# Optimization experiments

Hardware: AMD Instinct MI355X
Metric: run time of the kernel (lower is better)

The kernel has to match this reference:

```python
import jax, jax.numpy as jnp
import numpy as np

B, T, S, N, C, H = 2, 16, 256, 32, 3072, 24
D = C // H  # 128 head_dim
EPS = 1e-6


def _layernorm(x):
    # LayerNorm, elementwise_affine=False, eps=1e-6
    mu = jnp.mean(x, axis=-1, keepdims=True)
    var = jnp.mean(jnp.square(x - mu), axis=-1, keepdims=True)
    return (x - mu) * jax.lax.rsqrt(var + EPS)


def _rmsnorm(x, w):
    # RMSNorm with learnable weight, computed in fp32 (matches x.float() path)
    ms = jnp.mean(jnp.square(x), axis=-1, keepdims=True)
    return x * jax.lax.rsqrt(ms + EPS) * w


def setup_inputs() -> dict:
    key = jax.random.key(0)
    ks = jax.random.split(key, 8)
    f = lambda k, sh: jax.random.normal(k, sh, dtype=jnp.float32)
    sc = 1.0 / np.sqrt(C)
    return {
        "x": f(ks[0], (B, T * S, C)),
        "motion_vec": f(ks[1], (B, T, N, C)),
        "motion_mask": jax.random.uniform(ks[2], (B, T * S), dtype=jnp.float32),
        "w_kv": f(ks[3], (2 * C, C)) * sc,
        "b_kv": jnp.zeros((2 * C,), jnp.float32),
        "w_q": f(ks[4], (C, C)) * sc,
        "b_q": jnp.zeros((C,), jnp.float32),
        "w_o": f(ks[5], (C, C)) * sc,
        "b_o": jnp.zeros((C,), jnp.float32),
        "q_norm_w": jnp.ones((D,), jnp.float32),
        "k_norm_w": jnp.ones((D,), jnp.float32),
    }


def reference(x, motion_vec, motion_mask, w_kv, b_kv, w_q, b_q, w_o, b_o,
              q_norm_w, k_norm_w):
    x_motion = _layernorm(motion_vec)            # [B,T,N,C]
    x_feat = _layernorm(x)                       # [B,T*S,C]

    kv = x_motion @ w_kv.T + b_kv                # [B,T,N,2C]
    kv = kv.reshape(B, T, N, 2, H, D)
    k, v = kv[:, :, :, 0], kv[:, :, :, 1]        # [B,T,N,H,D]

    q = (x_feat @ w_q.T + b_q).reshape(B, T, S, H, D)
    q = _rmsnorm(q, q_norm_w)
    k = _rmsnorm(k, k_norm_w)

    # frame-local cross-attention: queries = spatial tokens, keys = motion tokens
    scale = 1.0 / jnp.sqrt(jnp.float32(D))
    scores = jnp.einsum('btshd,btnhd->bthsn', q, k) * scale  # [B,T,H,S,N]
    probs = jax.nn.softmax(scores, axis=-1)
    attn = jnp.einsum('bthsn,btnhd->btshd', probs, v)        # [B,T,S,H,D]
    attn = attn.reshape(B, T * S, C)

    out = attn @ w_o.T + b_o                     # [B,T*S,C]
    return out * motion_mask[:, :, None]
```

## Files before the change

kernel.cpp:

```cpp
#include <hip/hip_runtime.h>
#include <math.h>

typedef unsigned short u16;
typedef unsigned int u32;
typedef short bf16x8 __attribute__((ext_vector_type(8)));
typedef float f32x4 __attribute__((ext_vector_type(4)));
typedef u16 u16x4 __attribute__((ext_vector_type(4)));
typedef u16 u16x8 __attribute__((ext_vector_type(8)));
typedef u32 u32x4 __attribute__((ext_vector_type(4)));

static __device__ __forceinline__ float b2f(u16 u) {
  union { u32 i; float f; } v; v.i = ((u32)u) << 16; return v.f;
}
static __device__ __forceinline__ u16 f2b(float f) {
  union { float f; u32 i; } v; v.f = f;
  u32 r = v.i + 0x7fffu + ((v.i >> 16) & 1u);
  return (u16)(r >> 16);
}
static __device__ __forceinline__ void cvt16(const float* src, u16* dst, int i) {
  f32x4 v = *(const f32x4*)(src + (size_t)i * 4);
  u16x4 w; w.x = f2b(v.x); w.y = f2b(v.y); w.z = f2b(v.z); w.w = f2b(v.w);
  *(u16x4*)(dst + (size_t)i * 4) = w;
}

static __device__ __forceinline__ void g2l16(const void* g, void* l) {
  typedef __attribute__((address_space(1))) const void gvoid;
  typedef __attribute__((address_space(3))) void lvoid;
  __builtin_amdgcn_global_load_lds((gvoid*)g, (lvoid*)l, 16, 0, 0);
}

__global__ __launch_bounds__(256)
void wcvt_kernel(const float* __restrict__ src, u16* __restrict__ dst, int n4)
{
  for (int i = blockIdx.x * 256 + threadIdx.x; i < n4; i += gridDim.x * 256)
    cvt16(src, dst, i);
}

__global__ __launch_bounds__(256)
void prep_kernel(const float* __restrict__ x, const float* __restrict__ mv,
                 u16* __restrict__ xf, u16* __restrict__ xm,
                 const float* __restrict__ wq, u16* __restrict__ wqs,
                 const float* __restrict__ wkv, u16* __restrict__ wkvs)
{
  const int b = blockIdx.x, tid = threadIdx.x;
  if (b >= 9216) {
    if (b < 10240) {
      const int n4 = 3072 * 3072 / 4;
      for (int i = (b - 9216) * 256 + tid; i < n4; i += 1024 * 256) cvt16(wq, wqs, i);
    } else {
      const int n4 = 6144 * 3072 / 4;
      for (int i = (b - 10240) * 256 + tid; i < n4; i += 1024 * 256) cvt16(wkv, wkvs, i);
    }
    return;
  }
  const float* src; u16* dst;
  if (b < 8192) { src = x + (size_t)b * 3072;          dst = xf + (size_t)b * 3072; }
  else          { src = mv + (size_t)(b - 8192) * 3072; dst = xm + (size_t)(b - 8192) * 3072; }

  f32x4 vals[3];
  #pragma unroll
  for (int i = 0; i < 3; ++i) vals[i] = *(const f32x4*)(src + tid * 4 + i * 1024);

  float s1 = 0.f, s2 = 0.f;
  #pragma unroll
  for (int i = 0; i < 3; ++i) {
    f32x4 v = vals[i];
    s1 += v.x + v.y + v.z + v.w;
    s2 += v.x * v.x + v.y * v.y + v.z * v.z + v.w * v.w;
  }
  #pragma unroll
  for (int o = 32; o > 0; o >>= 1) { s1 += __shfl_down(s1, o); s2 += __shfl_down(s2, o); }
  __shared__ float r1[4], r2[4];
  const int wv = tid >> 6, ln = tid & 63;
  if (ln == 0) { r1[wv] = s1; r2[wv] = s2; }
  __syncthreads();
  const float t1 = r1[0] + r1[1] + r1[2] + r1[3];
  const float t2 = r2[0] + r2[1] + r2[2] + r2[3];
  const float mu = t1 * (1.f / 3072.f);
  const float rs = rsqrtf(t2 * (1.f / 3072.f) - mu * mu + 1e-6f);
  #pragma unroll
  for (int i = 0; i < 3; ++i) {
    f32x4 v = vals[i]; u16x4 w;
    w.x = f2b((v.x - mu) * rs); w.y = f2b((v.y - mu) * rs);
    w.z = f2b((v.z - mu) * rs); w.w = f2b((v.w - mu) * rs);
    *(u16x4*)(dst + tid * 4 + i * 1024) = w;
  }
}

template<int EPI, typename TOUT>
static __device__ __forceinline__ void g256_body(
    const u16* __restrict__ A, const u16* __restrict__ Wb,
    const float* __restrict__ bias, const float* __restrict__ mask,
    TOUT* __restrict__ C, int N, int K, int tb, u16* L)
{
  const int tid = threadIdx.x, wave = tid >> 6, lane = tid & 63;
  const int nbx = N >> 7;
  const int brow = (tb / nbx) << 8;
  const int bcol = (tb % nbx) << 7;
  const int wr = wave >> 1, wc = wave & 1;

  const u16* gA = A + (size_t)brow * K;
  const u16* gB = Wb + (size_t)bcol * K;

  const int srow = tid >> 2;
  const int scol = 8 * ((lane & 3) ^ ((lane >> 3) & 3));
  const int rcoff = 8 * ((lane >> 4) ^ ((lane >> 1) & 3));

  f32x4 acc[8][4] = {};

  auto STAGE = [&](int b, int tk) {
    u16* bufA = &L[b * 12288];
    u16* bufB = bufA + 8192;
    const u16* srcA = gA + tk + scol;
    const u16* srcB = gB + tk + scol;
    #pragma unroll
    for (int j = 0; j < 4; ++j)
      g2l16(srcA + (size_t)(j * 64 + srow) * K, bufA + (j * 64 + wave * 16) * 32);
    #pragma unroll
    for (int j = 0; j < 2; ++j)
      g2l16(srcB + (size_t)(j * 64 + srow) * K, bufB + (j * 64 + wave * 16) * 32);
  };

  auto COMPUTE = [&](int b) {
    const u16* bufA = &L[b * 12288];
    const u16* bufB = bufA + 8192;
    bf16x8 af[8], bfv[4];
    #pragma unroll
    for (int m = 0; m < 8; ++m)
      af[m] = *(const bf16x8*)&bufA[(wr * 128 + m * 16 + (lane & 15)) * 32 + rcoff];
    #pragma unroll
    for (int n = 0; n < 4; ++n)
      bfv[n] = *(const bf16x8*)&bufB[(wc * 64 + n * 16 + (lane & 15)) * 32 + rcoff];
    __builtin_amdgcn_s_setprio(1);
    #pragma unroll
    for (int m = 0; m < 8; ++m)
      #pragma unroll
      for (int n = 0; n < 4; ++n)
        acc[m][n] = __builtin_amdgcn_mfma_f32_16x16x32_bf16(af[m], bfv[n], acc[m][n], 0, 0, 0);
    __builtin_amdgcn_s_setprio(0);
  };

  STAGE(0, 0);
  STAGE(1, 32);
  asm volatile("s_waitcnt vmcnt(6)" ::: "memory");
  __builtin_amdgcn_s_barrier();
  __builtin_amdgcn_sched_barrier(0);

  const int NT = K >> 5;
  int cur = 0;
  for (int t = 0; t < NT; ++t) {
    const bool pf = (t + 2) < NT;
    if (pf) {
      int nb = cur + 2; if (nb >= 3) nb -= 3;
      STAGE(nb, (t + 2) << 5);
    }
    COMPUTE(cur);
    if (pf) asm volatile("s_waitcnt vmcnt(6)" ::: "memory");
    else    asm volatile("s_waitcnt vmcnt(0)" ::: "memory");
    __builtin_amdgcn_s_barrier();
    __builtin_amdgcn_sched_barrier(0);
    if (++cur == 3) cur = 0;
  }

  #pragma unroll
  for (int m = 0; m < 8; ++m) {
    const int row = brow + wr * 128 + m * 16 + ((lane >> 4) << 2);
    #pragma unroll
    for (int n = 0; n < 4; ++n) {
      const int col = bcol + wc * 64 + n * 16 + (lane & 15);
      const float bv = bias[col];
      #pragma unroll
      for (int i = 0; i < 4; ++i) {
        float v = acc[m][n][i] + bv;
        if (EPI == 1) v *= mask[row + i];
        if constexpr (__is_same(TOUT, u16))
          C[(size_t)(row + i) * N + col] = f2b(v);
        else
          C[(size_t)(row + i) * N + col] = v;
      }
    }
  }
}

template<int EPI, typename TOUT>
__global__ __launch_bounds__(256, 2)
void gemm256(const u16* __restrict__ A, const u16* __restrict__ Wb,
             const float* __restrict__ bias, const float* __restrict__ mask,
             TOUT* __restrict__ C, int M, int N, int K)
{
  __shared__ __align__(16) u16 L[36864];
  const int nwg = gridDim.x;
  const int tb = (blockIdx.x & 7) * (nwg >> 3) + (blockIdx.x >> 3);
  g256_body<EPI, TOUT>(A, Wb, bias, mask, C, N, K, tb, L);
}

__global__ __launch_bounds__(256, 2)
void gemm_fused(const u16* __restrict__ Aq, const u16* __restrict__ Bq,
                const float* __restrict__ bq, u16* __restrict__ Cq,
                const u16* __restrict__ Akv, const u16* __restrict__ Bkv,
                const float* __restrict__ bkv, u16* __restrict__ Ckv, int K)
{
  __shared__ __align__(16) u16 L[36864];
  const int b0 = blockIdx.x;
  if (b0 < 768) {
    const int tb = (b0 & 7) * 96 + (b0 >> 3);
    g256_body<0, u16>(Aq, Bq, bq, nullptr, Cq, 3072, K, tb, L);
  } else {
    const int b2 = b0 - 768;
    const int tb = (b2 & 7) * 24 + (b2 >> 3);
    g256_body<0, u16>(Akv, Bkv, bkv, nullptr, Ckv, 6144, K, tb, L);
  }
}

template<int EPI, typename TOUT>
__global__ __launch_bounds__(256, 2)
void gemm192(const u16* __restrict__ A, const u16* __restrict__ Wb,
             const float* __restrict__ bias, const float* __restrict__ mask,
             TOUT* __restrict__ C, int M, int N, int K)
{
  __shared__ __align__(16) u16 L[30720];
  const int tid = threadIdx.x, wave = tid >> 6, lane = tid & 63;
  const int nwg = gridDim.x;
  const int tb = (blockIdx.x & 7) * (nwg >> 3) + (blockIdx.x >> 3);
  const int nbx = N / 192;
  const int brow = (tb / nbx) << 7;
  const int bcol = (tb % nbx) * 192;
  const int wr = wave >> 1, wc = wave & 1;

  const u16* gA = A + (size_t)brow * K;
  const u16* gB = Wb + (size_t)bcol * K;

  const int srow = tid >> 2;
  const int scol = 8 * ((lane & 3) ^ ((lane >> 3) & 3));
  const int rcoff = 8 * ((lane >> 4) ^ ((lane >> 1) & 3));
  const int lr = lane & 15;

  f32x4 acc[4][6] = {};

  auto STAGE = [&](int b, int tk) {
    u16* bufA = &L[b * 10240];
    u16* bufB = bufA + 4096;
    const u16* srcA = gA + tk + scol;
    const u16* srcB = gB + tk + scol;
    #pragma unroll
    for (int j = 0; j < 2; ++j)
      g2l16(srcA + (size_t)(j * 64 + srow) * K, bufA + (j * 64 + wave * 16) * 32);
    #pragma unroll
    for (int j = 0; j < 3; ++j)
      g2l16(srcB + (size_t)(j * 64 + srow) * K, bufB + (j * 64 + wave * 16) * 32);
  };

  auto COMPUTE = [&](int b) {
    const u16* bufA = &L[b * 10240];
    const u16* bufB = bufA + 4096;
    bf16x8 af[4], bfv[6];
    #pragma unroll
    for (int m = 0; m < 4; ++m)
      af[m] = *(const bf16x8*)&bufA[(wr * 64 + m * 16 + lr) * 32 + rcoff];
    #pragma unroll
    for (int n = 0; n < 6; ++n)
      bfv[n] = *(const bf16x8*)&bufB[(wc * 96 + n * 16 + lr) * 32 + rcoff];
    __builtin_amdgcn_s_setprio(1);
    #pragma unroll
    for (int m = 0; m < 4; ++m)
      #pragma unroll
      for (int n = 0; n < 6; ++n)
        acc[m][n] = __builtin_amdgcn_mfma_f32_16x16x32_bf16(af[m], bfv[n], acc[m][n], 0, 0, 0);
    __builtin_amdgcn_s_setprio(0);
  };

  STAGE(0, 0);
  STAGE(1, 32);
  asm volatile("s_waitcnt vmcnt(5)" ::: "memory");
  __builtin_amdgcn_s_barrier();
  __builtin_amdgcn_sched_barrier(0);

  const int NT = K >> 5;
  int cur = 0;
  for (int t = 0; t < NT; ++t) {
    const bool pf = (t + 2) < NT;
    if (pf) {
      int nb = cur + 2; if (nb >= 3) nb -= 3;
      STAGE(nb, (t + 2) << 5);
    }
    COMPUTE(cur);
    if (pf) asm volatile("s_waitcnt vmcnt(5)" ::: "memory");
    else    asm volatile("s_waitcnt vmcnt(0)" ::: "memory");
    __builtin_amdgcn_s_barrier();
    __builtin_amdgcn_sched_barrier(0);
    if (++cur == 3) cur = 0;
  }

  #pragma unroll
  for (int m = 0; m < 4; ++m) {
    const int row = brow + wr * 64 + m * 16 + ((lane >> 4) << 2);
    #pragma unroll
    for (int n = 0; n < 6; ++n) {
      const int col = bcol + wc * 96 + n * 16 + lr;
      const float bv = bias[col];
      #pragma unroll
      for (int i = 0; i < 4; ++i) {
        float v = acc[m][n][i] + bv;
        if (EPI == 1) v *= mask[row + i];
        if constexpr (__is_same(TOUT, u16))
          C[(size_t)(row + i) * N + col] = f2b(v);
        else
          C[(size_t)(row + i) * N + col] = v;
      }
    }
  }
}

template<int EPI, typename TOUT>
__global__ __launch_bounds__(256)
void gemm_mixed(const u16* __restrict__ A, const float* __restrict__ W,
                const float* __restrict__ bias, const float* __restrict__ mask,
                TOUT* __restrict__ C, int M, int N, int K)
{
  __shared__ __align__(16) u16 lA[4096];
  __shared__ __align__(16) u16 lB[4096];
  const int tid = threadIdx.x, wave = tid >> 6, lane = tid & 63;
  const int nbx = N >> 7;
  const int brow = (blockIdx.x / nbx) << 7;
  const int bcol = (blockIdx.x % nbx) << 7;
  const int wr = wave >> 1, wc = wave & 1;

  f32x4 acc[4][4] = {};
  const u16* gA = A + (size_t)brow * K;
  const float* gB = W + (size_t)bcol * K;
  const int br = tid >> 1, bk0 = (tid & 1) << 4;
  const float* bsrc0 = gB + (size_t)br * K + bk0;
  u16* bdst = &lB[br * 32 + bk0];

  for (int tk = 0; tk < K; tk += 32) {
    #pragma unroll
    for (int j = 0; j < 2; ++j) {
      const int c = j * 256 + wave * 64 + lane;
      const int r = c >> 2, k8 = (c & 3) << 3;
      g2l16(gA + (size_t)r * K + tk + k8, (char*)lA + (size_t)(j * 256 + wave * 64) * 16);
    }
    {
      const float* src = bsrc0 + tk;
      #pragma unroll
      for (int j = 0; j < 4; ++j) {
        f32x4 v = *(const f32x4*)(src + 4 * j);
        u16x4 w; w.x = f2b(v.x); w.y = f2b(v.y); w.z = f2b(v.z); w.w = f2b(v.w);
        *(u16x4*)(bdst + 4 * j) = w;
      }
    }
    __syncthreads();

    bf16x8 af[4], bfr[4];
    #pragma unroll
    for (int m = 0; m < 4; ++m)
      af[m] = *(const bf16x8*)&lA[(wr * 64 + m * 16 + (lane & 15)) * 32 + ((lane >> 4) << 3)];
    #pragma unroll
    for (int n = 0; n < 4; ++n)
      bfr[n] = *(const bf16x8*)&lB[(wc * 64 + n * 16 + (lane & 15)) * 32 + ((lane >> 4) << 3)];
    #pragma unroll
    for (int m = 0; m < 4; ++m)
      #pragma unroll
      for (int n = 0; n < 4; ++n)
        acc[m][n] = __builtin_amdgcn_mfma_f32_16x16x32_bf16(af[m], bfr[n], acc[m][n], 0, 0, 0);
    __syncthreads();
  }

  #pragma unroll
  for (int m = 0; m < 4; ++m) {
    const int row = brow + wr * 64 + m * 16 + ((lane >> 4) << 2);
    #pragma unroll
    for (int n = 0; n < 4; ++n) {
      const int col = bcol + wc * 64 + n * 16 + (lane & 15);
      const float bv = bias[col];
      #pragma unroll
      for (int i = 0; i < 4; ++i) {
        float v = acc[m][n][i] + bv;
        if (EPI == 1) v *= mask[row + i];
        if constexpr (__is_same(TOUT, u16))
          C[(size_t)(row + i) * N + col] = f2b(v);
        else
          C[(size_t)(row + i) * N + col] = v;
      }
    }
  }
}

__global__ __launch_bounds__(256)
void attn_wcvt(const u16* __restrict__ qb, const u16* __restrict__ kvb,
               const float* __restrict__ qw, const float* __restrict__ kw,
               u16* __restrict__ attnb,
               const float* __restrict__ wo, u16* __restrict__ wos)
{
  __shared__ __align__(16) u16 Kn[32 * 136];
  __shared__ __align__(16) u16 Vt[128 * 40];
  __shared__ __align__(16) u16 Pl[256 * 40];
  __shared__ __align__(16) u16 Ol[4][16 * 136];
  const int tid = threadIdx.x;
  if (blockIdx.x >= 768) {
    const int n4 = 3072 * 3072 / 4;
    for (int i = (blockIdx.x - 768) * 256 + tid; i < n4; i += 1024 * 256)
      cvt16(wo, wos, i);
    return;
  }
  const int wave = tid >> 6, lane = tid & 63;
  const int h = blockIdx.x % 24;
  const int bt = blockIdx.x / 24;

  {
    const int n = tid >> 3, sub = tid & 7;
    const size_t base = (size_t)(bt * 32 + n) * 6144 + (size_t)h * 128;
    const u16* kp = kvb + base + sub * 16;
    u16x8 k0 = *(const u16x8*)kp;
    u16x8 k1 = *(const u16x8*)(kp + 8);
    float kv_[16]; float ss = 0.f;
    #pragma unroll
    for (int j = 0; j < 8; ++j) { kv_[j] = b2f(k0[j]); kv_[8 + j] = b2f(k1[j]); }
    #pragma unroll
    for (int j = 0; j < 16; ++j) ss += kv_[j] * kv_[j];
    ss += __shfl_xor(ss, 1); ss += __shfl_xor(ss, 2); ss += __shfl_xor(ss, 4);
    const float krs = rsqrtf(ss * (1.f / 128.f) + 1e-6f);
    u16x8 w0, w1;
    #pragma unroll
    for (int j = 0; j < 8; ++j) {
      const int d = sub * 16 + j;
      w0[j] = f2b(kv_[j] * krs * kw[d] * qw[d]);
      w1[j] = f2b(kv_[8 + j] * krs * kw[d + 8] * qw[d + 8]);
    }
    *(u16x8*)&Kn[n * 136 + sub * 16] = w0;
    *(u16x8*)&Kn[n * 136 + sub * 16 + 8] = w1;
  }
  {
    const int k = tid >> 3, dc = (tid & 7) * 16;
    const u16* vp = kvb + (size_t)(bt * 32 + k) * 6144 + (size_t)h * 128 + 3072 + dc;
    u16x8 v0 = *(const u16x8*)vp;
    u16x8 v1 = *(const u16x8*)(vp + 8);
    #pragma unroll
    for (int j = 0; j < 8; ++j) {
      Vt[(dc + j) * 40 + k] = v0[j];
      Vt[(dc + 8 + j) * 40 + k] = v1[j];
    }
  }
  __syncthreads();

  const int q0 = wave * 64;
  const int lr = lane & 15, lg = lane >> 4;

  for (int m = 0; m < 4; ++m) {
    const int qrow = q0 + m * 16 + lr;
    const u16* qp = qb + (size_t)(bt * 256 + qrow) * 3072 + (size_t)h * 128 + lg * 8;
    bf16x8 qf[4];
    #pragma unroll
    for (int k = 0; k < 4; ++k) qf[k] = *(const bf16x8*)(qp + k * 32);
    float ss = 0.f;
    #pragma unroll
    for (int k = 0; k < 4; ++k)
      #pragma unroll
      for (int j = 0; j < 8; ++j) { const float f = b2f((u16)qf[k][j]); ss += f * f; }
    ss += __shfl_xor(ss, 16); ss += __shfl_xor(ss, 32);
    const float qsc = rsqrtf(ss * (1.f / 128.f) + 1e-6f) * 0.08838834764831845f;
    #pragma unroll
    for (int k = 0; k < 4; ++k)
      #pragma unroll
      for (int j = 0; j < 8; ++j)
        qf[k][j] = (short)f2b(b2f((u16)qf[k][j]) * qsc);

    f32x4 s0 = {0.f, 0.f, 0.f, 0.f}, s1 = {0.f, 0.f, 0.f, 0.f};
    #pragma unroll
    for (int k = 0; k < 4; ++k) {
      bf16x8 kb0 = *(const bf16x8*)&Kn[(lr) * 136 + k * 32 + lg * 8];
      bf16x8 kb1 = *(const bf16x8*)&Kn[(16 + lr) * 136 + k * 32 + lg * 8];
      s0 = __builtin_amdgcn_mfma_f32_16x16x32_bf16(qf[k], kb0, s0, 0, 0, 0);
      s1 = __builtin_amdgcn_mfma_f32_16x16x32_bf16(qf[k], kb1, s1, 0, 0, 0);
    }

    float mx[4], sm[4], e0[4], e1[4];
    #pragma unroll
    for (int i = 0; i < 4; ++i) mx[i] = fmaxf(s0[i], s1[i]);
    #pragma unroll
    for (int o = 1; o <= 8; o <<= 1)
      #pragma unroll
      for (int i = 0; i < 4; ++i) mx[i] = fmaxf(mx[i], __shfl_xor(mx[i], o));
    #pragma unroll
    for (int i = 0; i < 4; ++i) {
      e0[i] = __expf(s0[i] - mx[i]);
      e1[i] = __expf(s1[i] - mx[i]);
      sm[i] = e0[i] + e1[i];
    }
    #pragma unroll
    for (int o = 1; o <= 8; o <<= 1)
      #pragma unroll
      for (int i = 0; i < 4; ++i) sm[i] += __shfl_xor(sm[i], o);
    #pragma unroll
    for (int i = 0; i < 4; ++i) {
      const float inv = 1.f / sm[i];
      const int pr = (q0 + m * 16 + lg * 4 + i) * 40;
      Pl[pr + lr] = f2b(e0[i] * inv);
      Pl[pr + 16 + lr] = f2b(e1[i] * inv);
    }
    asm volatile("s_waitcnt lgkmcnt(0)" ::: "memory");
    __builtin_amdgcn_sched_barrier(0);

    bf16x8 pf = *(const bf16x8*)&Pl[(q0 + m * 16 + lr) * 40 + lg * 8];
    f32x4 o_[8];
    #pragma unroll
    for (int n = 0; n < 8; ++n) {
      bf16x8 vb = *(const bf16x8*)&Vt[(n * 16 + lr) * 40 + lg * 8];
      o_[n] = __builtin_amdgcn_mfma_f32_16x16x32_bf16(
                pf, vb, (f32x4){0.f, 0.f, 0.f, 0.f}, 0, 0, 0);
    }

    u16* ow = &Ol[wave][0];
    #pragma unroll
    for (int n = 0; n < 8; ++n)
      #pragma unroll
      for (int i = 0; i < 4; ++i)
        ow[(lg * 4 + i) * 136 + n * 16 + lr] = f2b(o_[n][i]);
    asm volatile("s_waitcnt lgkmcnt(0)" ::: "memory");
    __builtin_amdgcn_sched_barrier(0);
    const int r = lane >> 2, cc = (lane & 3) * 32;
    u16* gout = attnb + (size_t)(bt * 256 + q0 + m * 16 + r) * 3072 + (size_t)h * 128 + cc;
    #pragma unroll
    for (int c = 0; c < 4; ++c)
      *(u16x8*)(gout + c * 8) = *(const u16x8*)&ow[r * 136 + cc + c * 8];
    asm volatile("s_waitcnt lgkmcnt(0)" ::: "memory");
    __builtin_amdgcn_sched_barrier(0);
  }
}

extern "C" void kernel_launch(void* const* d_in, const int* in_sizes, int n_in,
                              void* d_out, int out_size, void* d_ws, size_t ws_size,
                              hipStream_t stream) {
  const float* x    = (const float*)d_in[0];
  const float* mv   = (const float*)d_in[1];
  const float* mask = (const float*)d_in[2];
  const float* wkv  = (const float*)d_in[3];
  const float* bkv  = (const float*)d_in[4];
  const float* wq   = (const float*)d_in[5];
  const float* bq   = (const float*)d_in[6];
  const float* wo   = (const float*)d_in[7];
  const float* bo   = (const float*)d_in[8];
  const float* qnw  = (const float*)d_in[9];
  const float* knw  = (const float*)d_in[10];
  float* out = (float*)d_out;

  char* ws = (char*)d_ws;

  if (ws_size >= 176160768u) {
    u16* wqs  = (u16*)(ws);
    u16* wkvs = (u16*)(ws + 18874368);
    u16* xf   = (u16*)(ws + 56623104);
    u16* xm   = (u16*)(ws + 106954752);
    u16* qbuf = (u16*)(ws + 113246208);
    u16* kvb  = (u16*)(ws + 163577856);
    u16* wos  = wqs;

    prep_kernel<<<11264, 256, 0, stream>>>(x, mv, xf, xm, wq, wqs, wkv, wkvs);
    gemm_fused<<<960, 256, 0, stream>>>(xf, wqs, bq, qbuf, xm, wkvs, bkv, kvb, 3072);
    attn_wcvt<<<1792, 256, 0, stream>>>(qbuf, kvb, qnw, knw, xf, wo, wos);
    gemm192<1, float><<<1024, 256, 0, stream>>>(xf, wos, bo, mask, out, 8192, 3072, 3072);
  } else if (ws_size >= 157286400u) {
    u16* xf    = (u16*)(ws);
    u16* xm    = (u16*)(ws + 50331648);
    u16* qbuf  = (u16*)(ws + 56623104);
    u16* kvb   = (u16*)(ws + 106954752);
    u16* wslab = (u16*)(ws + 119537664);

    prep_kernel<<<9216, 256, 0, stream>>>(x, mv, xf, xm, wq, wslab, wkv, wslab);
    wcvt_kernel<<<2048, 256, 0, stream>>>(wq, wslab, 3072 * 3072 / 4);
    gemm256<0, u16><<<768, 256, 0, stream>>>(xf, wslab, bq, nullptr, qbuf, 8192, 3072, 3072);
    wcvt_kernel<<<2048, 256, 0, stream>>>(wkv, wslab, 6144 * 3072 / 4);
    gemm256<0, u16><<<192, 256, 0, stream>>>(xm, wslab, bkv, nullptr, kvb, 1024, 6144, 3072);
    attn_wcvt<<<768, 256, 0, stream>>>(qbuf, kvb, qnw, knw, xf, wo, wslab);
    wcvt_kernel<<<2048, 256, 0, stream>>>(wo, wslab, 3072 * 3072 / 4);
    gemm192<1, float><<<1024, 256, 0, stream>>>(xf, wslab, bo, mask, out, 8192, 3072, 3072);
  } else {
    u16* xf   = (u16*)(ws);
    u16* xm   = (u16*)(ws + 50331648);
    u16* qbuf = (u16*)(ws + 56623104);
    u16* kvb  = (u16*)(ws + 106954752);

    prep_kernel<<<9216, 256, 0, stream>>>(x, mv, xf, xm, wq, xf, wkv, xf);
    gemm_mixed<0, u16><<<1536, 256, 0, stream>>>(xf, wq, bq, nullptr, qbuf, 8192, 3072, 3072);
    gemm_mixed<0, u16><<<384, 256, 0, stream>>>(xm, wkv, bkv, nullptr, kvb, 1024, 6144, 3072);
    attn_wcvt<<<768, 256, 0, stream>>>(qbuf, kvb, qnw, knw, xf, wo, xf);
    gemm_mixed<1, float><<<1536, 256, 0, stream>>>(xf, wo, bo, mask, out, 8192, 3072, 3072);
  }
}
```

Before: 462.1 us.

## Add 8-wave 256x256 GEMM with ping-pong LDS pipeline for Q and output projections

Adds a new 512-thread GEMM kernel that computes 256x256 output tiles with 64-wide K steps and double-buffered LDS. Each K step is split into eight barrier-separated MFMA phases, and global prefetch is interleaved between them. It replaces the fused Q/KV GEMM and the 192-wide output GEMM, so the KV projection now launches as its own gemm256 kernel. The goals are more reuse per tile and better overlap of loads with MFMA; the costs are lower occupancy (one 128KB-LDS block per CU), many more barriers, and an extra kernel launch.

After: 496.7 us. 1.07x slower.

```diff
diff --git a/kernel.cpp b/kernel.cpp
--- a/kernel.cpp
+++ b/kernel.cpp
@@ -88,86 +88,139 @@
 }
 
 template<int EPI, typename TOUT>
-static __device__ __forceinline__ void g256_body(
-    const u16* __restrict__ A, const u16* __restrict__ Wb,
-    const float* __restrict__ bias, const float* __restrict__ mask,
-    TOUT* __restrict__ C, int N, int K, int tb, u16* L)
+__global__ __launch_bounds__(512, 1)
+void gemm8p(const u16* __restrict__ A, const u16* __restrict__ Wb,
+            const float* __restrict__ bias, const float* __restrict__ mask,
+            TOUT* __restrict__ C, int M, int N, int K)
 {
+  __shared__ __align__(16) u16 L[65536];
   const int tid = threadIdx.x, wave = tid >> 6, lane = tid & 63;
-  const int nbx = N >> 7;
-  const int brow = (tb / nbx) << 8;
-  const int bcol = (tb % nbx) << 7;
-  const int wr = wave >> 1, wc = wave & 1;
+  const int wr = wave >> 2, wc = wave & 3;
+  const int lr = lane & 15, lg = lane >> 4;
+
+  const int nwg = gridDim.x;
+  const int bid = (blockIdx.x & 7) * (nwg >> 3) + (blockIdx.x >> 3);
+  const int nbx = N >> 8;
+  const int brow = (bid / nbx) << 8;
+  const int bcol = (bid % nbx) << 8;
 
   const u16* gA = A + (size_t)brow * K;
   const u16* gB = Wb + (size_t)bcol * K;
 
-  const int srow = tid >> 2;
-  const int scol = 8 * ((lane & 3) ^ ((lane >> 3) & 3));
-  const int rcoff = 8 * ((lane >> 4) ^ ((lane >> 1) & 3));
+  const int sr = tid >> 3;
+  const int sc = 8 * ((tid & 7) ^ (sr & 7));
+  const int ch0 = 8 * (lg ^ (lr & 7));
+  const int ch1 = 8 * ((4 + lg) ^ (lr & 7));
 
   f32x4 acc[8][4] = {};
 
-  auto STAGE = [&](int b, int tk) {
-    u16* bufA = &L[b * 12288];
-    u16* bufB = bufA + 8192;
-    const u16* srcA = gA + tk + scol;
-    const u16* srcB = gB + tk + scol;
-    #pragma unroll
-    for (int j = 0; j < 4; ++j)
-      g2l16(srcA + (size_t)(j * 64 + srow) * K, bufA + (j * 64 + wave * 16) * 32);
-    #pragma unroll
-    for (int j = 0; j < 2; ++j)
-      g2l16(srcB + (size_t)(j * 64 + srow) * K, bufB + (j * 64 + wave * 16) * 32);
+  auto SG = [&](int sel, int d, int h, int T) {
+    const u16* g = (sel == 0 ? gA : gB) + (size_t)(h * 128 + sr) * K + T * 64 + sc;
+    u16* l = &L[sel * 32768 + (d * 2 + h) * 8192 + tid * 8];
+    g2l16(g, l);
+    g2l16(g + (size_t)64 * K, l + 4096);
   };
-
-  auto COMPUTE = [&](int b) {
-    const u16* bufA = &L[b * 12288];
-    const u16* bufB = bufA + 8192;
-    bf16x8 af[8], bfv[4];
-    #pragma unroll
-    for (int m = 0; m < 8; ++m)
-      af[m] = *(const bf16x8*)&bufA[(wr * 128 + m * 16 + (lane & 15)) * 32 + rcoff];
-    #pragma unroll
-    for (int n = 0; n < 4; ++n)
-      bfv[n] = *(const bf16x8*)&bufB[(wc * 64 + n * 16 + (lane & 15)) * 32 + rcoff];
-    __builtin_amdgcn_s_setprio(1);
-    #pragma unroll
-    for (int m = 0; m < 8; ++m)
-      #pragma unroll
-      for (int n = 0; n < 4; ++n)
-        acc[m][n] = __builtin_amdgcn_mfma_f32_16x16x32_bf16(af[m], bfv[n], acc[m][n], 0, 0, 0);
-    __builtin_amdgcn_s_setprio(0);
+  auto LDA = [&](int d, int mh, bf16x8 a[4][2]) {
+    const u16* base = &L[(d * 2 + wr) * 8192 + mh * 4096 + lr * 64];
+    #pragma unroll
+    for (int mm = 0; mm < 4; ++mm) {
+      a[mm][0] = *(const bf16x8*)&base[mm * 1024 + ch0];
+      a[mm][1] = *(const bf16x8*)&base[mm * 1024 + ch1];
+    }
   };
-
-  STAGE(0, 0);
-  STAGE(1, 32);
-  asm volatile("s_waitcnt vmcnt(6)" ::: "memory");
+  auto LDB = [&](int d, int nh, bf16x8 b[2][2]) {
+    const u16* base = &L[32768 + (d * 2 + (wc >> 1)) * 8192 + (wc & 1) * 4096 + nh * 2048 + lr * 64];
+    #pragma unroll
+    for (int nn = 0; nn < 2; ++nn) {
+      b[nn][0] = *(const bf16x8*)&base[nn * 1024 + ch0];
+      b[nn][1] = *(const bf16x8*)&base[nn * 1024 + ch1];
+    }
+  };
+
+#define MM8P(mh, nh, a, b)                                                     \
+  __builtin_amdgcn_s_setprio(1);                                               \
+  _Pragma("unroll")                                                            \
+  for (int mm = 0; mm < 4; ++mm)                                               \
+    _Pragma("unroll")                                                          \
+    for (int nn = 0; nn < 2; ++nn) {                                           \
+      acc[(mh)*4+mm][(nh)*2+nn] = __builtin_amdgcn_mfma_f32_16x16x32_bf16(     \
+          a[mm][0], b[nn][0], acc[(mh)*4+mm][(nh)*2+nn], 0, 0, 0);             \
+      acc[(mh)*4+mm][(nh)*2+nn] = __builtin_amdgcn_mfma_f32_16x16x32_bf16(     \
+          a[mm][1], b[nn][1], acc[(mh)*4+mm][(nh)*2+nn], 0, 0, 0);             \
+    }                                                                          \
+  __builtin_amdgcn_s_setprio(0);
+
+#define BAR_PRE()                                                              \
+  asm volatile("" ::: "memory");                                               \
+  __builtin_amdgcn_s_barrier();                                                \
+  asm volatile("s_waitcnt lgkmcnt(0)" ::: "memory");                           \
+  __builtin_amdgcn_sched_barrier(0);
+
+#define BAR_POST()                                                             \
+  asm volatile("" ::: "memory");                                               \
+  __builtin_amdgcn_s_barrier();                                                \
+  __builtin_amdgcn_sched_barrier(0);
+
+  SG(0, 0, 0, 0); SG(0, 0, 1, 0); SG(1, 0, 0, 0); SG(1, 0, 1, 0);
+  SG(0, 1, 0, 1);
+  asm volatile("s_waitcnt vmcnt(2)" ::: "memory");
   __builtin_amdgcn_s_barrier();
   __builtin_amdgcn_sched_barrier(0);
 
-  const int NT = K >> 5;
-  int cur = 0;
-  for (int t = 0; t < NT; ++t) {
-    const bool pf = (t + 2) < NT;
-    if (pf) {
-      int nb = cur + 2; if (nb >= 3) nb -= 3;
-      STAGE(nb, (t + 2) << 5);
-    }
-    COMPUTE(cur);
-    if (pf) asm volatile("s_waitcnt vmcnt(6)" ::: "memory");
-    else    asm volatile("s_waitcnt vmcnt(0)" ::: "memory");
-    __builtin_amdgcn_s_barrier();
-    __builtin_amdgcn_sched_barrier(0);
-    if (++cur == 3) cur = 0;
-  }
+  const int NI = K >> 7;
+  for (int i = 0; i < NI; ++i) {
+    const int t = 2 * i;
+    const bool pf = (i + 1) < NI;
+    bf16x8 a[4][2], b[2][2];
+
+    LDA(0, 0, a); LDB(0, 0, b);
+    SG(0, 1, 1, t + 1);
+    BAR_PRE(); MM8P(0, 0, a, b); BAR_POST();
+
+    LDB(0, 1, b);
+    SG(1, 1, 0, t + 1);
+    BAR_PRE(); MM8P(0, 1, a, b); BAR_POST();
+
+    LDA(0, 1, a);
+    SG(1, 1, 1, t + 1);
+    BAR_PRE(); MM8P(1, 1, a, b); BAR_POST();
+
+    LDB(0, 0, b);
+    if (pf) SG(0, 0, 0, t + 2);
+    BAR_PRE(); MM8P(1, 0, a, b);
+    if (pf) { asm volatile("s_waitcnt vmcnt(2)" ::: "memory"); }
+    else    { asm volatile("s_waitcnt vmcnt(0)" ::: "memory"); }
+    BAR_POST();
+
+    LDA(1, 0, a); LDB(1, 0, b);
+    if (pf) SG(0, 0, 1, t + 2);
+    BAR_PRE(); MM8P(0, 0, a, b); BAR_POST();
+
+    LDB(1, 1, b);
+    if (pf) SG(1, 0, 0, t + 2);
+    BAR_PRE(); MM8P(0, 1, a, b); BAR_POST();
+
+    LDA(1, 1, a);
+    if (pf) SG(1, 0, 1, t + 2);
+    BAR_PRE(); MM8P(1, 1, a, b); BAR_POST();
+
+    LDB(1, 0, b);
+    if (pf) SG(0, 1, 0, t + 3);
+    BAR_PRE(); MM8P(1, 0, a, b);
+    if (pf) { asm volatile("s_waitcnt vmcnt(2)" ::: "memory"); }
+    BAR_POST();
+  }
+
+#undef MM8P
+#undef BAR_PRE
+#undef BAR_POST
 
   #pragma unroll
   for (int m = 0; m < 8; ++m) {
-    const int row = brow + wr * 128 + m * 16 + ((lane >> 4) << 2);
+    const int row = brow + wr * 128 + m * 16 + (lg << 2);
     #pragma unroll
     for (int n = 0; n < 4; ++n) {
-      const int col = bcol + wc * 64 + n * 16 + (lane & 15);
+      const int col = bcol + wc * 64 + n * 16 + lr;
       const float bv = bias[col];
       #pragma unroll
       for (int i = 0; i < 4; ++i) {
@@ -189,42 +242,13 @@
              TOUT* __restrict__ C, int M, int N, int K)
 {
   __shared__ __align__(16) u16 L[36864];
+  const int tid = threadIdx.x, wave = tid >> 6, lane = tid & 63;
+
   const int nwg = gridDim.x;
-  const int tb = (blockIdx.x & 7) * (nwg >> 3) + (blockIdx.x >> 3);
-  g256_body<EPI, TOUT>(A, Wb, bias, mask, C, N, K, tb, L);
-}
-
-__global__ __launch_bounds__(256, 2)
-void gemm_fused(const u16* __restrict__ Aq, const u16* __restrict__ Bq,
-                const float* __restrict__ bq, u16* __restrict__ Cq,
-                const u16* __restrict__ Akv, const u16* __restrict__ Bkv,
-                const float* __restrict__ bkv, u16* __restrict__ Ckv, int K)
-{
-  __shared__ __align__(16) u16 L[36864];
-  const int b0 = blockIdx.x;
-  if (b0 < 768) {
-    const int tb = (b0 & 7) * 96 + (b0 >> 3);
-    g256_body<0, u16>(Aq, Bq, bq, nullptr, Cq, 3072, K, tb, L);
-  } else {
-    const int b2 = b0 - 768;
-    const int tb = (b2 & 7) * 24 + (b2 >> 3);
-    g256_body<0, u16>(Akv, Bkv, bkv, nullptr, Ckv, 6144, K, tb, L);
-  }
-}
-
-template<int EPI, typename TOUT>
-__global__ __launch_bounds__(256, 2)
-void gemm192(const u16* __restrict__ A, const u16* __restrict__ Wb,
-             const float* __restrict__ bias, const float* __restrict__ mask,
-             TOUT* __restrict__ C, int M, int N, int K)
-{
-  __shared__ __align__(16) u16 L[30720];
-  const int tid = threadIdx.x, wave = tid >> 6, lane = tid & 63;
-  const int nwg = gridDim.x;
-  const int tb = (blockIdx.x & 7) * (nwg >> 3) + (blockIdx.x >> 3);
-  const int nbx = N / 192;
-  const int brow = (tb / nbx) << 7;
-  const int bcol = (tb % nbx) * 192;
+  const int bid = (blockIdx.x & 7) * (nwg >> 3) + (blockIdx.x >> 3);
+  const int nbx = N >> 7;
+  const int brow = (bid / nbx) << 8;
+  const int bcol = (bid % nbx) << 7;
   const int wr = wave >> 1, wc = wave & 1;
 
   const u16* gA = A + (size_t)brow * K;
@@ -233,45 +257,44 @@
   const int srow = tid >> 2;
   const int scol = 8 * ((lane & 3) ^ ((lane >> 3) & 3));
   const int rcoff = 8 * ((lane >> 4) ^ ((lane >> 1) & 3));
-  const int lr = lane & 15;
-
-  f32x4 acc[4][6] = {};
+
+  f32x4 acc[8][4] = {};
 
   auto STAGE = [&](int b, int tk) {
-    u16* bufA = &L[b * 10240];
-    u16* bufB = bufA + 4096;
+    u16* bufA = &L[b * 12288];
+    u16* bufB = bufA + 8192;
     const u16* srcA = gA + tk + scol;
     const u16* srcB = gB + tk + scol;
     #pragma unroll
+    for (int j = 0; j < 4; ++j)
+      g2l16(srcA + (size_t)(j * 64 + srow) * K, bufA + (j * 64 + wave * 16) * 32);
+    #pragma unroll
     for (int j = 0; j < 2; ++j)
-      g2l16(srcA + (size_t)(j * 64 + srow) * K, bufA + (j * 64 + wave * 16) * 32);
-    #pragma unroll
-    for (int j = 0; j < 3; ++j)
       g2l16(srcB + (size_t)(j * 64 + srow) * K, bufB + (j * 64 + wave * 16) * 32);
   };
 
   auto COMPUTE = [&](int b) {
-    const u16* bufA = &L[b * 10240];
-    const u16* bufB = bufA + 4096;
-    bf16x8 af[4], bfv[6];
-    #pragma unroll
-    for (int m = 0; m < 4; ++m)
-      af[m] = *(const bf16x8*)&bufA[(wr * 64 + m * 16 + lr) * 32 + rcoff];
-    #pragma unroll
-    for (int n = 0; n < 6; ++n)
-      bfv[n] = *(const bf16x8*)&bufB[(wc * 96 + n * 16 + lr) * 32 + rcoff];
+    const u16* bufA = &L[b * 12288];
+    const u16* bufB = bufA + 8192;
+    bf16x8 af[8], bfv[4];
+    #pragma unroll
+    for (int m = 0; m < 8; ++m)
+      af[m] = *(const bf16x8*)&bufA[(wr * 128 + m * 16 + (lane & 15)) * 32 + rcoff];
+    #pragma unroll
+    for (int n = 0; n < 4; ++n)
+      bfv[n] = *(const bf16x8*)&bufB[(wc * 64 + n * 16 + (lane & 15)) * 32 + rcoff];
     __builtin_amdgcn_s_setprio(1);
     #pragma unroll
-    for (int m = 0; m < 4; ++m)
-      #pragma unroll
-      for (int n = 0; n < 6; ++n)
+    for (int m = 0; m < 8; ++m)
+      #pragma unroll
+      for (int n = 0; n < 4; ++n)
         acc[m][n] = __builtin_amdgcn_mfma_f32_16x16x32_bf16(af[m], bfv[n], acc[m][n], 0, 0, 0);
     __builtin_amdgcn_s_setprio(0);
   };
 
   STAGE(0, 0);
   STAGE(1, 32);
-  asm volatile("s_waitcnt vmcnt(5)" ::: "memory");
+  asm volatile("s_waitcnt vmcnt(6)" ::: "memory");
   __builtin_amdgcn_s_barrier();
   __builtin_amdgcn_sched_barrier(0);
 
@@ -284,7 +307,7 @@
       STAGE(nb, (t + 2) << 5);
     }
     COMPUTE(cur);
-    if (pf) asm volatile("s_waitcnt vmcnt(5)" ::: "memory");
+    if (pf) asm volatile("s_waitcnt vmcnt(6)" ::: "memory");
     else    asm volatile("s_waitcnt vmcnt(0)" ::: "memory");
     __builtin_amdgcn_s_barrier();
     __builtin_amdgcn_sched_barrier(0);
@@ -292,11 +315,11 @@
   }
 
   #pragma unroll
-  for (int m = 0; m < 4; ++m) {
-    const int row = brow + wr * 64 + m * 16 + ((lane >> 4) << 2);
-    #pragma unroll
-    for (int n = 0; n < 6; ++n) {
-      const int col = bcol + wc * 96 + n * 16 + lr;
+  for (int m = 0; m < 8; ++m) {
+    const int row = brow + wr * 128 + m * 16 + ((lane >> 4) << 2);
+    #pragma unroll
+    for (int n = 0; n < 4; ++n) {
+      const int col = bcol + wc * 64 + n * 16 + (lane & 15);
       const float bv = bias[col];
       #pragma unroll
       for (int i = 0; i < 4; ++i) {
@@ -555,9 +578,10 @@
     u16* wos  = wqs;
 
     prep_kernel<<<11264, 256, 0, stream>>>(x, mv, xf, xm, wq, wqs, wkv, wkvs);
-    gemm_fused<<<960, 256, 0, stream>>>(xf, wqs, bq, qbuf, xm, wkvs, bkv, kvb, 3072);
+    gemm8p<0, u16><<<384, 512, 0, stream>>>(xf, wqs, bq, nullptr, qbuf, 8192, 3072, 3072);
+    gemm256<0, u16><<<192, 256, 0, stream>>>(xm, wkvs, bkv, nullptr, kvb, 1024, 6144, 3072);
     attn_wcvt<<<1792, 256, 0, stream>>>(qbuf, kvb, qnw, knw, xf, wo, wos);
-    gemm192<1, float><<<1024, 256, 0, stream>>>(xf, wos, bo, mask, out, 8192, 3072, 3072);
+    gemm8p<1, float><<<384, 512, 0, stream>>>(xf, wos, bo, mask, out, 8192, 3072, 3072);
   } else if (ws_size >= 157286400u) {
     u16* xf    = (u16*)(ws);
     u16* xm    = (u16*)(ws + 50331648);
@@ -567,12 +591,12 @@
 
     prep_kernel<<<9216, 256, 0, stream>>>(x, mv, xf, xm, wq, wslab, wkv, wslab);
     wcvt_kernel<<<2048, 256, 0, stream>>>(wq, wslab, 3072 * 3072 / 4);
-    gemm256<0, u16><<<768, 256, 0, stream>>>(xf, wslab, bq, nullptr, qbuf, 8192, 3072, 3072);
+    gemm8p<0, u16><<<384, 512, 0, stream>>>(xf, wslab, bq, nullptr, qbuf, 8192, 3072, 3072);
     wcvt_kernel<<<2048, 256, 0, stream>>>(wkv, wslab, 6144 * 3072 / 4);
     gemm256<0, u16><<<192, 256, 0, stream>>>(xm, wslab, bkv, nullptr, kvb, 1024, 6144, 3072);
     attn_wcvt<<<768, 256, 0, stream>>>(qbuf, kvb, qnw, knw, xf, wo, wslab);
     wcvt_kernel<<<2048, 256, 0, stream>>>(wo, wslab, 3072 * 3072 / 4);
-    gemm192<1, float><<<1024, 256, 0, stream>>>(xf, wslab, bo, mask, out, 8192, 3072, 3072);
+    gemm8p<1, float><<<384, 512, 0, stream>>>(xf, wslab, bo, mask, out, 8192, 3072, 3072);
   } else {
     u16* xf   = (u16*)(ws);
     u16* xm   = (u16*)(ws + 50331648);
```
